# Optimization experiments

Measured on AMD Instinct MI355X. Metric: run time of the kernel, lower is better.

Reference implementation:

```python
import jax, jax.numpy as jnp
import numpy as np

N, E, F_IN, H, C, L = 50000, 800000, 128, 128, 47, 3
BN_EPS = 1e-5


def setup_inputs() -> dict:
    key = jax.random.key(0)
    ks = jax.random.split(key, 12)
    s = 0.1
    return {
        "x": jax.random.normal(ks[0], (N, F_IN), jnp.float32),
        "edge_index": jax.random.randint(ks[1], (2, E), 0, N, jnp.int32),
        # stacked GINConv MLP params (in_channels == hidden so all layers stack)
        "W1": jax.random.normal(ks[2], (L, F_IN, H), jnp.float32) * s,
        "b1": jnp.full((L, H), 0.01, jnp.float32),
        "gamma": jnp.ones((L, H), jnp.float32),
        "beta": jnp.zeros((L, H), jnp.float32),
        "bn_mean": jnp.zeros((L, H), jnp.float32),
        "bn_var": jnp.ones((L, H), jnp.float32),
        "W2": jax.random.normal(ks[3], (L, H, H), jnp.float32) * s,
        "b2": jnp.full((L, H), 0.01, jnp.float32),
        # head
        "lw1": jax.random.normal(ks[4], (H, H), jnp.float32) * s,
        "lb1": jnp.zeros((H,), jnp.float32),
        "lw2": jax.random.normal(ks[5], (H, C), jnp.float32) * s,
        "lb2": jnp.zeros((C,), jnp.float32),
    }


def reference(x, edge_index, W1, b1, gamma, beta, bn_mean, bn_var, W2, b2, lw1, lb1, lw2, lb2):
    src, dst = edge_index[0], edge_index[1]
    h = x
    for i in range(L):
        # GINConv: nn((1 + eps) * x + sum_{j in N(i)} x_j), eps = 0
        agg = jax.ops.segment_sum(h[src], dst, num_segments=N)  # [N, H] scatter-sum
        z = agg + h
        z = z @ W1[i] + b1[i]
        # BatchNorm1d in eval mode (running stats)
        z = (z - bn_mean[i]) * jax.lax.rsqrt(bn_var[i] + BN_EPS) * gamma[i] + beta[i]
        z = jax.nn.relu(z)
        h = jax.nn.relu(z @ W2[i] + b2[i])
    h = jax.nn.relu(h @ lw1 + lb1)
    # dropout disabled (eval mode)
    logits = h @ lw2 + lb2
    return jax.nn.log_softmax(logits, axis=-1)
```

## Files before the change

### kernel.cpp

```cpp
#include <hip/hip_runtime.h>
#include <math.h>

#define NN 50000
#define EE 800000
#define HH 128
#define LL 3
#define CC 47
#define CAP 64
#define FILL_B 2048
#define NT_TILES 782
#define PS ((size_t)(NN + 1) * 64)

typedef _Float16 half8 __attribute__((ext_vector_type(8)));
typedef float    f32x4 __attribute__((ext_vector_type(4)));
typedef float    f32x2 __attribute__((ext_vector_type(2)));
typedef unsigned int   u32x2 __attribute__((ext_vector_type(2)));
typedef unsigned short us8 __attribute__((ext_vector_type(8)));

__device__ __forceinline__ f32x4 mfma16(half8 a, half8 b, f32x4 c) {
    return __builtin_amdgcn_mfma_f32_16x16x32_f16(a, b, c, 0, 0, 0);
}

__device__ __forceinline__ void acc8_from_fp8(u32x2 w, float* a) {
    f32x2 p0 = __builtin_amdgcn_cvt_pk_f32_fp8(w[0], false);
    f32x2 p1 = __builtin_amdgcn_cvt_pk_f32_fp8(w[0], true);
    f32x2 p2 = __builtin_amdgcn_cvt_pk_f32_fp8(w[1], false);
    f32x2 p3 = __builtin_amdgcn_cvt_pk_f32_fp8(w[1], true);
    a[0] += p0[0]; a[1] += p0[1]; a[2] += p1[0]; a[3] += p1[1];
    a[4] += p2[0]; a[5] += p2[1]; a[6] += p3[0]; a[7] += p3[1];
}
__device__ __forceinline__ u32x2 pack8_fp8(const float* z) {
    unsigned int lo = __builtin_amdgcn_cvt_pk_fp8_f32(z[0], z[1], 0, false);
    lo = (unsigned int)__builtin_amdgcn_cvt_pk_fp8_f32(z[2], z[3], (int)lo, true);
    unsigned int hi = __builtin_amdgcn_cvt_pk_fp8_f32(z[4], z[5], 0, false);
    hi = (unsigned int)__builtin_amdgcn_cvt_pk_fp8_f32(z[6], z[7], (int)hi, true);
    u32x2 w; w[0] = lo; w[1] = hi;
    return w;
}

__global__ void k_fill_prep(const int* __restrict__ ei, int* __restrict__ cursor,
                            unsigned short* __restrict__ csr,
                            const float* __restrict__ x, const float* __restrict__ W1,
                            const float* __restrict__ W2, const float* __restrict__ lw1,
                            const float* __restrict__ lw2, const float* __restrict__ b1,
                            const float* __restrict__ gamma, const float* __restrict__ beta,
                            const float* __restrict__ bnm, const float* __restrict__ bnv,
                            unsigned char* __restrict__ x8, unsigned char* __restrict__ h8a,
                            unsigned char* __restrict__ h8b, _Float16* __restrict__ Wt1h,
                            _Float16* __restrict__ Wt2h, _Float16* __restrict__ lw1t,
                            _Float16* __restrict__ lw2t, float* __restrict__ A1f,
                            float* __restrict__ B1f) {
    if (blockIdx.x < FILL_B) {
        const int part = blockIdx.x & 7;
        const int chunk = blockIdx.x >> 3;
        const int nchunks = FILL_B >> 3;
        const int lo = part * (NN / 8);
        const int hi = (part == 7) ? NN : lo + (NN / 8);
        for (int e = chunk * 256 + threadIdx.x; e < EE; e += nchunks * 256) {
            const int d = ei[EE + e];
            if (d >= lo && d < hi) {
                const int pos = atomicAdd(&cursor[d], 1);
                if (pos < CAP) csr[(d << 6) + pos] = (unsigned short)ei[e];
            }
        }
        return;
    }
    const int i = (blockIdx.x - FILL_B) * 256 + threadIdx.x;
    const int Q0 = (NN * HH) / 8;
    const int Q1 = Q0 + LL * HH * HH;
    const int Q2 = Q1 + LL * HH * HH;
    const int Q3 = Q2 + HH * HH;
    const int Q4 = Q3 + 48 * HH;
    const int Q5 = Q4 + LL * HH;
    const int Q6 = Q5 + 3 * HH;
    if (i < Q0) {
        const int node = i >> 4, fg = i & 15;
        const f32x4* xp = (const f32x4*)(x + (size_t)node * HH + fg * 8);
        f32x4 u = xp[0], v = xp[1];
        float z[8] = {u[0], u[1], u[2], u[3], v[0], v[1], v[2], v[3]};
        const int plane = fg >> 3, po = (fg & 7) * 8;
        *(u32x2*)(x8 + (size_t)plane * PS + (size_t)node * 64 + po) = pack8_fp8(z);
    } else if (i < Q1) {
        int j = i - Q0;
        int l = j / (HH * HH);
        int n = (j / HH) % HH;
        int k = j % HH;
        Wt1h[l * HH * HH + n * HH + k] = (_Float16)W1[l * HH * HH + k * HH + n];
    } else if (i < Q2) {
        int j = i - Q1;
        int l = j / (HH * HH);
        int n = (j / HH) % HH;
        int k = j % HH;
        Wt2h[l * HH * HH + n * HH + k] = (_Float16)W2[l * HH * HH + k * HH + n];
    } else if (i < Q3) {
        int j = i - Q2;
        int n = j / HH, k = j % HH;
        lw1t[n * HH + k] = (_Float16)lw1[k * HH + n];
    } else if (i < Q4) {
        int j = i - Q3;
        int n = j / HH, k = j % HH;
        lw2t[n * HH + k] = (_Float16)((n < CC) ? lw2[k * CC + n] : 0.f);
    } else if (i < Q5) {
        int j = i - Q4;
        float s = gamma[j] * rsqrtf(bnv[j] + 1e-5f);
        A1f[j] = s;
        B1f[j] = (b1[j] - bnm[j]) * s + beta[j];
    } else if (i < Q6) {
        int j = i - Q5;
        int b = j >> 7, k = j & 127;
        unsigned char* t = (b == 0) ? x8 : ((b == 1) ? h8a : h8b);
        t[(size_t)(k >> 6) * PS + (size_t)NN * 64 + (k & 63)] = 0;
    }
}

__device__ __forceinline__ void gather_tile8(
    const unsigned char* __restrict__ hin8, const int* __restrict__ degs,
    const unsigned short* __restrict__ csr, _Float16* Ab, int tile0, int tid) {
    const int fo8 = (tid & 7) * 8;
    const int nd = tid >> 3;
#pragma unroll
    for (int plane = 0; plane < 2; ++plane) {
        const unsigned char* hp = hin8 + (size_t)plane * PS;
#pragma unroll
        for (int pass = 0; pass < 2; ++pass) {
            const int r = pass * 32 + nd;
            const int g = tile0 + r;
            const int gg = (g < NN) ? g : NN;
            float a[8] = {0.f, 0.f, 0.f, 0.f, 0.f, 0.f, 0.f, 0.f};
            u32x2 hv = *(const u32x2*)(hp + (size_t)gg * 64 + fo8);
            acc8_from_fp8(hv, a);
            int d = (g < NN) ? degs[g] : 0;
            d = (d < CAP) ? d : CAP;
            const unsigned short* crow = csr + (gg << 6);
            for (int kk = 0; kk < d; kk += 8) {
                us8 sv = *(const us8*)(crow + kk);
                int s[8];
#pragma unroll
                for (int j = 0; j < 8; ++j) s[j] = (kk + j < d) ? (int)sv[j] : NN;
                u32x2 v[8];
#pragma unroll
                for (int j = 0; j < 8; ++j) v[j] = *(const u32x2*)(hp + (size_t)s[j] * 64 + fo8);
#pragma unroll
                for (int j = 0; j < 8; ++j) acc8_from_fp8(v[j], a);
            }
            half8 o;
#pragma unroll
            for (int j = 0; j < 8; ++j) o[j] = (_Float16)a[j];
            *(half8*)(Ab + r * 136 + plane * 64 + fo8) = o;
        }
    }
}

__device__ __forceinline__ void store_tile8(
    unsigned char* __restrict__ hout8, const _Float16* Ab, int tile0, int tid) {
    const int fo8 = (tid & 7) * 8;
    const int nd = tid >> 3;
#pragma unroll
    for (int plane = 0; plane < 2; ++plane)
#pragma unroll
        for (int pass = 0; pass < 2; ++pass) {
            const int r = pass * 32 + nd;
            const int g = tile0 + r;
            if (g < NN) {
                half8 z = *(const half8*)(Ab + r * 136 + plane * 64 + fo8);
                float zf[8];
#pragma unroll
                for (int j = 0; j < 8; ++j) zf[j] = (float)z[j];
                *(u32x2*)(hout8 + (size_t)plane * PS + (size_t)g * 64 + fo8) = pack8_fp8(zf);
            }
        }
}

__global__ __launch_bounds__(256, 4) void k_layer(
    const unsigned char* __restrict__ hin8, unsigned char* __restrict__ hout8,
    const _Float16* __restrict__ Wt1, const _Float16* __restrict__ Wt2,
    const float* __restrict__ A1, const float* __restrict__ B1,
    const float* __restrict__ b2, const int* __restrict__ degs,
    const unsigned short* __restrict__ csr) {
    __shared__ _Float16 Ab[64 * 136];
    const int tid = threadIdx.x;
    const int wave = tid >> 6, lane = tid & 63;
    const int q = lane >> 4, l15 = lane & 15;
    const int tile0 = blockIdx.x * 64;

    half8 Bf[2][4];
#pragma unroll
    for (int t = 0; t < 2; ++t)
#pragma unroll
        for (int kt = 0; kt < 4; ++kt)
            Bf[t][kt] = *(const half8*)(Wt1 + (wave * 32 + t * 16 + l15) * 128 + kt * 32 + q * 8);

    gather_tile8(hin8, degs, csr, Ab, tile0, tid);
    __syncthreads();

    f32x4 acc[4][2];
#pragma unroll
    for (int s = 0; s < 4; ++s)
#pragma unroll
        for (int t = 0; t < 2; ++t) acc[s][t] = (f32x4){0.f, 0.f, 0.f, 0.f};
#pragma unroll
    for (int kt = 0; kt < 4; ++kt) {
        const int ko = kt * 32 + q * 8;
        half8 a0 = *(const half8*)(Ab + (0 * 16 + l15) * 136 + ko);
        half8 a1 = *(const half8*)(Ab + (1 * 16 + l15) * 136 + ko);
        half8 a2 = *(const half8*)(Ab + (2 * 16 + l15) * 136 + ko);
        half8 a3 = *(const half8*)(Ab + (3 * 16 + l15) * 136 + ko);
        acc[0][0] = mfma16(a0, Bf[0][kt], acc[0][0]);
        acc[1][0] = mfma16(a1, Bf[0][kt], acc[1][0]);
        acc[2][0] = mfma16(a2, Bf[0][kt], acc[2][0]);
        acc[3][0] = mfma16(a3, Bf[0][kt], acc[3][0]);
        acc[0][1] = mfma16(a0, Bf[1][kt], acc[0][1]);
        acc[1][1] = mfma16(a1, Bf[1][kt], acc[1][1]);
        acc[2][1] = mfma16(a2, Bf[1][kt], acc[2][1]);
        acc[3][1] = mfma16(a3, Bf[1][kt], acc[3][1]);
    }
#pragma unroll
    for (int t = 0; t < 2; ++t)
#pragma unroll
        for (int kt = 0; kt < 4; ++kt)
            Bf[t][kt] = *(const half8*)(Wt2 + (wave * 32 + t * 16 + l15) * 128 + kt * 32 + q * 8);
    __syncthreads();

#pragma unroll
    for (int t = 0; t < 2; ++t) {
        const int col = wave * 32 + t * 16 + l15;
        const float sc = A1[col], sh = B1[col];
#pragma unroll
        for (int s = 0; s < 4; ++s)
#pragma unroll
            for (int r = 0; r < 4; ++r) {
                const int row = s * 16 + q * 4 + r;
                float v = acc[s][t][r] * sc + sh;
                Ab[row * 136 + col] = (_Float16)fmaxf(v, 0.f);
            }
    }
    __syncthreads();

#pragma unroll
    for (int s = 0; s < 4; ++s)
#pragma unroll
        for (int t = 0; t < 2; ++t) acc[s][t] = (f32x4){0.f, 0.f, 0.f, 0.f};
#pragma unroll
    for (int kt = 0; kt < 4; ++kt) {
        const int ko = kt * 32 + q * 8;
        half8 a0 = *(const half8*)(Ab + (0 * 16 + l15) * 136 + ko);
        half8 a1 = *(const half8*)(Ab + (1 * 16 + l15) * 136 + ko);
        half8 a2 = *(const half8*)(Ab + (2 * 16 + l15) * 136 + ko);
        half8 a3 = *(const half8*)(Ab + (3 * 16 + l15) * 136 + ko);
        acc[0][0] = mfma16(a0, Bf[0][kt], acc[0][0]);
        acc[1][0] = mfma16(a1, Bf[0][kt], acc[1][0]);
        acc[2][0] = mfma16(a2, Bf[0][kt], acc[2][0]);
        acc[3][0] = mfma16(a3, Bf[0][kt], acc[3][0]);
        acc[0][1] = mfma16(a0, Bf[1][kt], acc[0][1]);
        acc[1][1] = mfma16(a1, Bf[1][kt], acc[1][1]);
        acc[2][1] = mfma16(a2, Bf[1][kt], acc[2][1]);
        acc[3][1] = mfma16(a3, Bf[1][kt], acc[3][1]);
    }
    __syncthreads();

#pragma unroll
    for (int t = 0; t < 2; ++t) {
        const int col = wave * 32 + t * 16 + l15;
        const float bb = b2[col];
#pragma unroll
        for (int s = 0; s < 4; ++s)
#pragma unroll
            for (int r = 0; r < 4; ++r) {
                const int row = s * 16 + q * 4 + r;
                Ab[row * 136 + col] = (_Float16)fmaxf(acc[s][t][r] + bb, 0.f);
            }
    }
    __syncthreads();

    store_tile8(hout8, Ab, tile0, tid);
}

__global__ __launch_bounds__(256, 4) void k_layer_head(
    const unsigned char* __restrict__ hin8,
    const _Float16* __restrict__ Wt1, const _Float16* __restrict__ Wt2,
    const float* __restrict__ A1, const float* __restrict__ B1,
    const float* __restrict__ b2,
    const _Float16* __restrict__ lw1t, const _Float16* __restrict__ lw2t,
    const float* __restrict__ lb1, const float* __restrict__ lb2,
    float* __restrict__ out, const int* __restrict__ degs,
    const unsigned short* __restrict__ csr) {
    __shared__ _Float16 Ab[64 * 136];
    const int tid = threadIdx.x;
    const int wave = tid >> 6, lane = tid & 63;
    const int q = lane >> 4, l15 = lane & 15;
    const int tile0 = blockIdx.x * 64;

    half8 Bf[2][4];
#pragma unroll
    for (int t = 0; t < 2; ++t)
#pragma unroll
        for (int kt = 0; kt < 4; ++kt)
            Bf[t][kt] = *(const half8*)(Wt1 + (wave * 32 + t * 16 + l15) * 128 + kt * 32 + q * 8);

    gather_tile8(hin8, degs, csr, Ab, tile0, tid);
    __syncthreads();

    f32x4 acc[4][2];
#pragma unroll
    for (int s = 0; s < 4; ++s)
#pragma unroll
        for (int t = 0; t < 2; ++t) acc[s][t] = (f32x4){0.f, 0.f, 0.f, 0.f};
#pragma unroll
    for (int kt = 0; kt < 4; ++kt) {
        const int ko = kt * 32 + q * 8;
        half8 a0 = *(const half8*)(Ab + (0 * 16 + l15) * 136 + ko);
        half8 a1 = *(const half8*)(Ab + (1 * 16 + l15) * 136 + ko);
        half8 a2 = *(const half8*)(Ab + (2 * 16 + l15) * 136 + ko);
        half8 a3 = *(const half8*)(Ab + (3 * 16 + l15) * 136 + ko);
        acc[0][0] = mfma16(a0, Bf[0][kt], acc[0][0]);
        acc[1][0] = mfma16(a1, Bf[0][kt], acc[1][0]);
        acc[2][0] = mfma16(a2, Bf[0][kt], acc[2][0]);
        acc[3][0] = mfma16(a3, Bf[0][kt], acc[3][0]);
        acc[0][1] = mfma16(a0, Bf[1][kt], acc[0][1]);
        acc[1][1] = mfma16(a1, Bf[1][kt], acc[1][1]);
        acc[2][1] = mfma16(a2, Bf[1][kt], acc[2][1]);
        acc[3][1] = mfma16(a3, Bf[1][kt], acc[3][1]);
    }
#pragma unroll
    for (int t = 0; t < 2; ++t)
#pragma unroll
        for (int kt = 0; kt < 4; ++kt)
            Bf[t][kt] = *(const half8*)(Wt2 + (wave * 32 + t * 16 + l15) * 128 + kt * 32 + q * 8);
    __syncthreads();
#pragma unroll
    for (int t = 0; t < 2; ++t) {
        const int col = wave * 32 + t * 16 + l15;
        const float sc = A1[col], sh = B1[col];
#pragma unroll
        for (int s = 0; s < 4; ++s)
#pragma unroll
            for (int r = 0; r < 4; ++r) {
                const int row = s * 16 + q * 4 + r;
                float v = acc[s][t][r] * sc + sh;
                Ab[row * 136 + col] = (_Float16)fmaxf(v, 0.f);
            }
    }
    __syncthreads();

#pragma unroll
    for (int s = 0; s < 4; ++s)
#pragma unroll
        for (int t = 0; t < 2; ++t) acc[s][t] = (f32x4){0.f, 0.f, 0.f, 0.f};
#pragma unroll
    for (int kt = 0; kt < 4; ++kt) {
        const int ko = kt * 32 + q * 8;
        half8 a0 = *(const half8*)(Ab + (0 * 16 + l15) * 136 + ko);
        half8 a1 = *(const half8*)(Ab + (1 * 16 + l15) * 136 + ko);
        half8 a2 = *(const half8*)(Ab + (2 * 16 + l15) * 136 + ko);
        half8 a3 = *(const half8*)(Ab + (3 * 16 + l15) * 136 + ko);
        acc[0][0] = mfma16(a0, Bf[0][kt], acc[0][0]);
        acc[1][0] = mfma16(a1, Bf[0][kt], acc[1][0]);
        acc[2][0] = mfma16(a2, Bf[0][kt], acc[2][0]);
        acc[3][0] = mfma16(a3, Bf[0][kt], acc[3][0]);
        acc[0][1] = mfma16(a0, Bf[1][kt], acc[0][1]);
        acc[1][1] = mfma16(a1, Bf[1][kt], acc[1][1]);
        acc[2][1] = mfma16(a2, Bf[1][kt], acc[2][1]);
        acc[3][1] = mfma16(a3, Bf[1][kt], acc[3][1]);
    }
#pragma unroll
    for (int t = 0; t < 2; ++t)
#pragma unroll
        for (int kt = 0; kt < 4; ++kt)
            Bf[t][kt] = *(const half8*)(lw1t + (wave * 32 + t * 16 + l15) * 128 + kt * 32 + q * 8);
    __syncthreads();
#pragma unroll
    for (int t = 0; t < 2; ++t) {
        const int col = wave * 32 + t * 16 + l15;
        const float bb = b2[col];
#pragma unroll
        for (int s = 0; s < 4; ++s)
#pragma unroll
            for (int r = 0; r < 4; ++r) {
                const int row = s * 16 + q * 4 + r;
                Ab[row * 136 + col] = (_Float16)fmaxf(acc[s][t][r] + bb, 0.f);
            }
    }
    __syncthreads();

#pragma unroll
    for (int s = 0; s < 4; ++s)
#pragma unroll
        for (int t = 0; t < 2; ++t) acc[s][t] = (f32x4){0.f, 0.f, 0.f, 0.f};
#pragma unroll
    for (int kt = 0; kt < 4; ++kt) {
        const int ko = kt * 32 + q * 8;
        half8 a0 = *(const half8*)(Ab + (0 * 16 + l15) * 136 + ko);
        half8 a1 = *(const half8*)(Ab + (1 * 16 + l15) * 136 + ko);
        half8 a2 = *(const half8*)(Ab + (2 * 16 + l15) * 136 + ko);
        half8 a3 = *(const half8*)(Ab + (3 * 16 + l15) * 136 + ko);
        acc[0][0] = mfma16(a0, Bf[0][kt], acc[0][0]);
        acc[1][0] = mfma16(a1, Bf[0][kt], acc[1][0]);
        acc[2][0] = mfma16(a2, Bf[0][kt], acc[2][0]);
        acc[3][0] = mfma16(a3, Bf[0][kt], acc[3][0]);
        acc[0][1] = mfma16(a0, Bf[1][kt], acc[0][1]);
        acc[1][1] = mfma16(a1, Bf[1][kt], acc[1][1]);
        acc[2][1] = mfma16(a2, Bf[1][kt], acc[2][1]);
        acc[3][1] = mfma16(a3, Bf[1][kt], acc[3][1]);
    }
    half8 Bh[4];
    if (wave < 3) {
#pragma unroll
        for (int kt = 0; kt < 4; ++kt)
            Bh[kt] = *(const half8*)(lw2t + (wave * 16 + l15) * 128 + kt * 32 + q * 8);
    }
    __syncthreads();
#pragma unroll
    for (int t = 0; t < 2; ++t) {
        const int col = wave * 32 + t * 16 + l15;
        const float bb = lb1[col];
#pragma unroll
        for (int s = 0; s < 4; ++s)
#pragma unroll
            for (int r = 0; r < 4; ++r) {
                const int row = s * 16 + q * 4 + r;
                Ab[row * 136 + col] = (_Float16)fmaxf(acc[s][t][r] + bb, 0.f);
            }
    }
    __syncthreads();

    f32x4 acc2[4];
#pragma unroll
    for (int s = 0; s < 4; ++s) acc2[s] = (f32x4){0.f, 0.f, 0.f, 0.f};
    if (wave < 3) {
#pragma unroll
        for (int kt = 0; kt < 4; ++kt) {
            const int ko = kt * 32 + q * 8;
            half8 a0 = *(const half8*)(Ab + (0 * 16 + l15) * 136 + ko);
            half8 a1 = *(const half8*)(Ab + (1 * 16 + l15) * 136 + ko);
            half8 a2 = *(const half8*)(Ab + (2 * 16 + l15) * 136 + ko);
            half8 a3 = *(const half8*)(Ab + (3 * 16 + l15) * 136 + ko);
            acc2[0] = mfma16(a0, Bh[kt], acc2[0]);
            acc2[1] = mfma16(a1, Bh[kt], acc2[1]);
            acc2[2] = mfma16(a2, Bh[kt], acc2[2]);
            acc2[3] = mfma16(a3, Bh[kt], acc2[3]);
        }
    }
    __syncthreads();

    float* Lb = (float*)Ab;
    if (wave < 3) {
        const int col = wave * 16 + l15;
        const float bb = (col < CC) ? lb2[col] : 0.f;
#pragma unroll
        for (int s = 0; s < 4; ++s)
#pragma unroll
            for (int r = 0; r < 4; ++r) {
                const int row = s * 16 + q * 4 + r;
                Lb[row * 49 + col] = acc2[s][r] + bb;
            }
    }
    __syncthreads();

    if (tid < 64) {
        const int g = tile0 + tid;
        if (g < NN) {
            float mx = -1e30f;
            for (int c = 0; c < CC; ++c) mx = fmaxf(mx, Lb[tid * 49 + c]);
            float ssum = 0.f;
            for (int c = 0; c < CC; ++c) ssum += expf(Lb[tid * 49 + c] - mx);
            const float ls = logf(ssum) + mx;
            for (int c = 0; c < CC; ++c) out[(size_t)g * CC + c] = Lb[tid * 49 + c] - ls;
        }
    }
}

extern "C" void kernel_launch(void* const* d_in, const int* in_sizes, int n_in,
                              void* d_out, int out_size, void* d_ws, size_t ws_size,
                              hipStream_t stream) {
    const float* x     = (const float*)d_in[0];
    const int*   ei    = (const int*)d_in[1];
    const float* W1    = (const float*)d_in[2];
    const float* b1    = (const float*)d_in[3];
    const float* gamma = (const float*)d_in[4];
    const float* beta  = (const float*)d_in[5];
    const float* bnm   = (const float*)d_in[6];
    const float* bnv   = (const float*)d_in[7];
    const float* W2    = (const float*)d_in[8];
    const float* b2    = (const float*)d_in[9];
    const float* lw1   = (const float*)d_in[10];
    const float* lb1   = (const float*)d_in[11];
    const float* lw2   = (const float*)d_in[12];
    const float* lb2   = (const float*)d_in[13];
    float* out = (float*)d_out;

    char* p = (char*)d_ws;
    auto carve = [&](size_t bytes) -> char* {
        char* r = p;
        p += (bytes + 255) & ~(size_t)255;
        return r;
    };
    int* cursor = (int*)carve((size_t)NN * 4);
    unsigned short* csr = (unsigned short*)carve((size_t)(NN + 1) * CAP * 2);
    _Float16* Wt1h = (_Float16*)carve((size_t)LL * HH * HH * 2);
    _Float16* Wt2h = (_Float16*)carve((size_t)LL * HH * HH * 2);
    _Float16* lw1t = (_Float16*)carve((size_t)HH * HH * 2);
    _Float16* lw2t = (_Float16*)carve((size_t)48 * HH * 2);
    float* A1f = (float*)carve((size_t)LL * HH * 4);
    float* B1f = (float*)carve((size_t)LL * HH * 4);
    unsigned char* x8  = (unsigned char*)carve((size_t)(NN + 1) * HH);
    unsigned char* h8a = (unsigned char*)carve((size_t)(NN + 1) * HH);
    unsigned char* h8b = (unsigned char*)carve((size_t)(NN + 1) * HH);

    hipMemsetAsync(cursor, 0, (size_t)NN * 4, stream);
    const int prep_total = (NN * HH) / 8 + 2 * LL * HH * HH + HH * HH + 48 * HH + LL * HH + 3 * HH;
    const int prep_blocks = (prep_total + 255) / 256;
    k_fill_prep<<<FILL_B + prep_blocks, 256, 0, stream>>>(
        ei, cursor, csr, x, W1, W2, lw1, lw2, b1, gamma, beta, bnm, bnv,
        x8, h8a, h8b, Wt1h, Wt2h, lw1t, lw2t, A1f, B1f);

    k_layer<<<NT_TILES, 256, 0, stream>>>(x8, h8a, Wt1h, Wt2h, A1f, B1f, b2,
                                          cursor, csr);
    k_layer<<<NT_TILES, 256, 0, stream>>>(h8a, h8b, Wt1h + HH * HH, Wt2h + HH * HH,
                                          A1f + HH, B1f + HH, b2 + HH,
                                          cursor, csr);
    k_layer_head<<<NT_TILES, 256, 0, stream>>>(h8b, Wt1h + 2 * HH * HH, Wt2h + 2 * HH * HH,
                                               A1f + 2 * HH, B1f + 2 * HH, b2 + 2 * HH,
                                               lw1t, lw2t, lb1, lb2, out,
                                               cursor, csr);
}
```

Measured before the change: 237.3 us.

## Store fp8 node features row-contiguous and gather 16 bytes per lane

The fp8 feature buffers move from two 64-byte planes per node to a single contiguous 128-byte row. Each gather lane now loads 16 bytes per neighbor in one pass instead of 8 bytes per plane over two passes. This halves the number of neighbor-index loops and the CSR index reads, and each neighbor row arrives in one contiguous 128-byte access. In exchange each lane holds 16 accumulators and 8 wide loads in flight, which raises register pressure under the 4-blocks-per-SM launch bound.

```diff
diff --git a/kernel.cpp b/kernel.cpp
--- a/kernel.cpp
+++ b/kernel.cpp
@@ -9,25 +9,26 @@
 #define CAP 64
 #define FILL_B 2048
 #define NT_TILES 782
-#define PS ((size_t)(NN + 1) * 64)
 
 typedef _Float16 half8 __attribute__((ext_vector_type(8)));
 typedef float    f32x4 __attribute__((ext_vector_type(4)));
 typedef float    f32x2 __attribute__((ext_vector_type(2)));
 typedef unsigned int   u32x2 __attribute__((ext_vector_type(2)));
+typedef unsigned int   u32x4 __attribute__((ext_vector_type(4)));
 typedef unsigned short us8 __attribute__((ext_vector_type(8)));
 
 __device__ __forceinline__ f32x4 mfma16(half8 a, half8 b, f32x4 c) {
     return __builtin_amdgcn_mfma_f32_16x16x32_f16(a, b, c, 0, 0, 0);
 }
 
-__device__ __forceinline__ void acc8_from_fp8(u32x2 w, float* a) {
-    f32x2 p0 = __builtin_amdgcn_cvt_pk_f32_fp8(w[0], false);
-    f32x2 p1 = __builtin_amdgcn_cvt_pk_f32_fp8(w[0], true);
-    f32x2 p2 = __builtin_amdgcn_cvt_pk_f32_fp8(w[1], false);
-    f32x2 p3 = __builtin_amdgcn_cvt_pk_f32_fp8(w[1], true);
-    a[0] += p0[0]; a[1] += p0[1]; a[2] += p1[0]; a[3] += p1[1];
-    a[4] += p2[0]; a[5] += p2[1]; a[6] += p3[0]; a[7] += p3[1];
+__device__ __forceinline__ void acc16_from_fp8(u32x4 w, float* a) {
+#pragma unroll
+    for (int i = 0; i < 4; ++i) {
+        f32x2 lo = __builtin_amdgcn_cvt_pk_f32_fp8(w[i], false);
+        f32x2 hi = __builtin_amdgcn_cvt_pk_f32_fp8(w[i], true);
+        a[i * 4 + 0] += lo[0]; a[i * 4 + 1] += lo[1];
+        a[i * 4 + 2] += hi[0]; a[i * 4 + 3] += hi[1];
+    }
 }
 __device__ __forceinline__ u32x2 pack8_fp8(const float* z) {
     unsigned int lo = __builtin_amdgcn_cvt_pk_fp8_f32(z[0], z[1], 0, false);
@@ -35,6 +36,16 @@
     unsigned int hi = __builtin_amdgcn_cvt_pk_fp8_f32(z[4], z[5], 0, false);
     hi = (unsigned int)__builtin_amdgcn_cvt_pk_fp8_f32(z[6], z[7], (int)hi, true);
     u32x2 w; w[0] = lo; w[1] = hi;
+    return w;
+}
+__device__ __forceinline__ u32x4 pack16_fp8(const float* z) {
+    u32x4 w;
+#pragma unroll
+    for (int i = 0; i < 4; ++i) {
+        unsigned int t = __builtin_amdgcn_cvt_pk_fp8_f32(z[i * 4 + 0], z[i * 4 + 1], 0, false);
+        t = (unsigned int)__builtin_amdgcn_cvt_pk_fp8_f32(z[i * 4 + 2], z[i * 4 + 3], (int)t, true);
+        w[i] = t;
+    }
     return w;
 }
 
@@ -74,12 +85,10 @@
     const int Q5 = Q4 + LL * HH;
     const int Q6 = Q5 + 3 * HH;
     if (i < Q0) {
-        const int node = i >> 4, fg = i & 15;
-        const f32x4* xp = (const f32x4*)(x + (size_t)node * HH + fg * 8);
+        const f32x4* xp = (const f32x4*)x + (size_t)i * 2;
         f32x4 u = xp[0], v = xp[1];
         float z[8] = {u[0], u[1], u[2], u[3], v[0], v[1], v[2], v[3]};
-        const int plane = fg >> 3, po = (fg & 7) * 8;
-        *(u32x2*)(x8 + (size_t)plane * PS + (size_t)node * 64 + po) = pack8_fp8(z);
+        ((u32x2*)x8)[i] = pack8_fp8(z);
     } else if (i < Q1) {
         int j = i - Q0;
         int l = j / (HH * HH);
@@ -109,66 +118,63 @@
         int j = i - Q5;
         int b = j >> 7, k = j & 127;
         unsigned char* t = (b == 0) ? x8 : ((b == 1) ? h8a : h8b);
-        t[(size_t)(k >> 6) * PS + (size_t)NN * 64 + (k & 63)] = 0;
+        t[(size_t)NN * HH + k] = 0;
     }
 }
 
 __device__ __forceinline__ void gather_tile8(
     const unsigned char* __restrict__ hin8, const int* __restrict__ degs,
     const unsigned short* __restrict__ csr, _Float16* Ab, int tile0, int tid) {
-    const int fo8 = (tid & 7) * 8;
+    const int fo16 = (tid & 7) * 16;
     const int nd = tid >> 3;
 #pragma unroll
-    for (int plane = 0; plane < 2; ++plane) {
-        const unsigned char* hp = hin8 + (size_t)plane * PS;
-#pragma unroll
-        for (int pass = 0; pass < 2; ++pass) {
-            const int r = pass * 32 + nd;
-            const int g = tile0 + r;
-            const int gg = (g < NN) ? g : NN;
-            float a[8] = {0.f, 0.f, 0.f, 0.f, 0.f, 0.f, 0.f, 0.f};
-            u32x2 hv = *(const u32x2*)(hp + (size_t)gg * 64 + fo8);
-            acc8_from_fp8(hv, a);
-            int d = (g < NN) ? degs[g] : 0;
-            d = (d < CAP) ? d : CAP;
-            const unsigned short* crow = csr + (gg << 6);
-            for (int kk = 0; kk < d; kk += 8) {
-                us8 sv = *(const us8*)(crow + kk);
-                int s[8];
-#pragma unroll
-                for (int j = 0; j < 8; ++j) s[j] = (kk + j < d) ? (int)sv[j] : NN;
-                u32x2 v[8];
-#pragma unroll
-                for (int j = 0; j < 8; ++j) v[j] = *(const u32x2*)(hp + (size_t)s[j] * 64 + fo8);
-#pragma unroll
-                for (int j = 0; j < 8; ++j) acc8_from_fp8(v[j], a);
-            }
-            half8 o;
-#pragma unroll
-            for (int j = 0; j < 8; ++j) o[j] = (_Float16)a[j];
-            *(half8*)(Ab + r * 136 + plane * 64 + fo8) = o;
+    for (int pass = 0; pass < 2; ++pass) {
+        const int r = pass * 32 + nd;
+        const int g = tile0 + r;
+        const int gg = (g < NN) ? g : NN;
+        float a[16] = {0.f, 0.f, 0.f, 0.f, 0.f, 0.f, 0.f, 0.f,
+                       0.f, 0.f, 0.f, 0.f, 0.f, 0.f, 0.f, 0.f};
+        u32x4 hv = *(const u32x4*)(hin8 + (size_t)gg * HH + fo16);
+        acc16_from_fp8(hv, a);
+        int d = (g < NN) ? degs[g] : 0;
+        d = (d < CAP) ? d : CAP;
+        const unsigned short* crow = csr + (gg << 6);
+        for (int kk = 0; kk < d; kk += 8) {
+            us8 sv = *(const us8*)(crow + kk);
+            int s[8];
+#pragma unroll
+            for (int j = 0; j < 8; ++j) s[j] = (kk + j < d) ? (int)sv[j] : NN;
+            u32x4 v[8];
+#pragma unroll
+            for (int j = 0; j < 8; ++j) v[j] = *(const u32x4*)(hin8 + (size_t)s[j] * HH + fo16);
+#pragma unroll
+            for (int j = 0; j < 8; ++j) acc16_from_fp8(v[j], a);
         }
+        half8 o0, o1;
+#pragma unroll
+        for (int j = 0; j < 8; ++j) { o0[j] = (_Float16)a[j]; o1[j] = (_Float16)a[8 + j]; }
+        *(half8*)(Ab + r * 136 + fo16) = o0;
+        *(half8*)(Ab + r * 136 + fo16 + 8) = o1;
     }
 }
 
 __device__ __forceinline__ void store_tile8(
     unsigned char* __restrict__ hout8, const _Float16* Ab, int tile0, int tid) {
-    const int fo8 = (tid & 7) * 8;
+    const int fo16 = (tid & 7) * 16;
     const int nd = tid >> 3;
 #pragma unroll
-    for (int plane = 0; plane < 2; ++plane)
-#pragma unroll
-        for (int pass = 0; pass < 2; ++pass) {
-            const int r = pass * 32 + nd;
-            const int g = tile0 + r;
-            if (g < NN) {
-                half8 z = *(const half8*)(Ab + r * 136 + plane * 64 + fo8);
-                float zf[8];
-#pragma unroll
-                for (int j = 0; j < 8; ++j) zf[j] = (float)z[j];
-                *(u32x2*)(hout8 + (size_t)plane * PS + (size_t)g * 64 + fo8) = pack8_fp8(zf);
-            }
+    for (int pass = 0; pass < 2; ++pass) {
+        const int r = pass * 32 + nd;
+        const int g = tile0 + r;
+        if (g < NN) {
+            half8 z0 = *(const half8*)(Ab + r * 136 + fo16);
+            half8 z1 = *(const half8*)(Ab + r * 136 + fo16 + 8);
+            float zf[16];
+#pragma unroll
+            for (int j = 0; j < 8; ++j) { zf[j] = (float)z0[j]; zf[8 + j] = (float)z1[j]; }
+            *(u32x4*)(hout8 + (size_t)g * HH + fo16) = pack16_fp8(zf);
         }
+    }
 }
 
 __global__ __launch_bounds__(256, 4) void k_layer(
```

Result: slower. 361.9 us (+52.5%).
